# Performance work log

Measured on AMD Instinct MI355X. Metric: run time of the kernel, lower is better.

The kernel has to match this reference:

```python
import jax, jax.numpy as jnp
import numpy as np

B, S, D, H, P = 4, 2048, 1024, 16, 10
DK = D // H

def setup_inputs() -> dict:
    key = jax.random.key(0)
    ks = jax.random.split(key, 12)
    inp = {
        'q': jax.random.normal(ks[0], (B, S, D), jnp.float32),
        'k': jax.random.normal(ks[1], (B, S, D), jnp.float32),
        'v': jax.random.normal(ks[2], (B, S, D), jnp.float32),
        # causal mask, broadcastable over batch/heads
        'mask': jnp.tril(jnp.ones((S, S), jnp.int32))[None, None, :, :],
        'Wq': jax.random.normal(ks[3], (D, D), jnp.float32) * (1.0 / np.sqrt(D)),
        'bq': jnp.zeros((D,), jnp.float32),
        'Wk': jax.random.normal(ks[4], (D, D), jnp.float32) * (1.0 / np.sqrt(D)),
        'bk': jnp.zeros((D,), jnp.float32),
        'Wv': jax.random.normal(ks[5], (D, D), jnp.float32) * (1.0 / np.sqrt(D)),
        'bv': jnp.zeros((D,), jnp.float32),
        'Wo': jax.random.normal(ks[6], (D, D), jnp.float32) * (1.0 / np.sqrt(D)),
        'bo': jnp.zeros((D,), jnp.float32),
        'prefix_k': jax.random.normal(ks[7], (H, P, DK), jnp.float32) * 0.02,
        'prefix_v': jax.random.normal(ks[8], (H, P, DK), jnp.float32) * 0.02,
    }
    return inp

def reference(q, k, v, mask, Wq, bq, Wk, bk, Wv, bv, Wo, bo, prefix_k, prefix_v):
    bs, sq, d = q.shape
    h, p, dk = prefix_k.shape
    # projections -> [B, H, S, dk]
    Q = (q @ Wq + bq).reshape(bs, sq, h, dk).transpose(0, 2, 1, 3)
    K = (k @ Wk + bk).reshape(bs, -1, h, dk).transpose(0, 2, 1, 3)
    V = (v @ Wv + bv).reshape(bs, -1, h, dk).transpose(0, 2, 1, 3)
    # prepend learnable prefix K/V along the key axis
    pK = jnp.broadcast_to(prefix_k[None], (bs, h, p, dk))
    pV = jnp.broadcast_to(prefix_v[None], (bs, h, p, dk))
    K = jnp.concatenate([pK, K], axis=2)  # [B,H,P+S,dk]
    V = jnp.concatenate([pV, V], axis=2)
    # extend mask: prefix positions always visible
    pref_mask = jnp.ones(mask.shape[:3] + (p,), mask.dtype)
    full_mask = jnp.concatenate([pref_mask, mask], axis=-1)  # [.,.,S,P+S]
    scores = jnp.einsum('bhqd,bhkd->bhqk', Q, K) / np.sqrt(dk).astype(jnp.float32)
    scores = jnp.where(full_mask == 0, jnp.asarray(-1e9, scores.dtype), scores)
    attn = jax.nn.softmax(scores, axis=-1)  # dropout in eval mode: identity
    out = jnp.einsum('bhqk,bhkd->bhqd', attn, V)
    out = out.transpose(0, 2, 1, 3).reshape(bs, sq, d)
    return out @ Wo + bo
```

## Files before the change

kernel.cpp:

```cpp
#include <hip/hip_runtime.h>

typedef __bf16 bf16x8 __attribute__((ext_vector_type(8)));
typedef __bf16 bf16x4 __attribute__((ext_vector_type(4)));
typedef float f32x4 __attribute__((ext_vector_type(4)));

constexpr int Sq = 2048, Dd = 1024, Hn = 16, Pn = 10, DK = 64;
constexpr int SKPAD = 2112;
constexpr int NBH = 64;
constexpr float LOG2E = 1.44269504088896340736f;

__device__ __forceinline__ float exp2_fast(float x) {
  return __builtin_amdgcn_exp2f(x);
}

__device__ __forceinline__ unsigned short f2bf(float f) {
  unsigned int u = __float_as_uint(f);
  u += 0x7fffu + ((u >> 16) & 1u);
  return (unsigned short)(u >> 16);
}

__device__ __forceinline__ void gload_lds16(const void* g, void* l) {
  __builtin_amdgcn_global_load_lds(
      (const __attribute__((address_space(1))) void*)g,
      (__attribute__((address_space(3))) void*)l, 16, 0, 0);
}

__device__ __forceinline__ f32x4 mfma16(bf16x8 a, bf16x8 b, f32x4 c) {
  return __builtin_amdgcn_mfma_f32_16x16x32_bf16(a, b, c, 0, 0, 0);
}

__global__ void k_wt(const float* __restrict__ W0, const float* __restrict__ W1,
                     const float* __restrict__ W2, const float* __restrict__ W3,
                     unsigned short* __restrict__ T0, unsigned short* __restrict__ T1,
                     unsigned short* __restrict__ T2, unsigned short* __restrict__ T3) {
  __shared__ float tile[32][33];
  const float* W; unsigned short* T;
  switch (blockIdx.z) {
    case 0: W = W0; T = T0; break;
    case 1: W = W1; T = T1; break;
    case 2: W = W2; T = T2; break;
    default: W = W3; T = T3; break;
  }
  int n0 = blockIdx.x * 32, k0 = blockIdx.y * 32;
  int tx = threadIdx.x, ty = threadIdx.y;
  for (int r = ty; r < 32; r += 8)
    tile[r][tx] = W[(size_t)(k0 + r) * Dd + n0 + tx];
  __syncthreads();
  for (int r = ty; r < 32; r += 8)
    T[(size_t)(n0 + r) * Dd + k0 + tx] = f2bf(tile[tx][r]);
}

__global__ void k_fill(const float* __restrict__ pk, const float* __restrict__ pv,
                       unsigned short* __restrict__ Kb, unsigned short* __restrict__ Vt) {
  int bh = blockIdx.x;
  int h = bh & (Hn - 1);
  unsigned short* Kbh = Kb + (size_t)bh * SKPAD * DK;
  unsigned short* Vth = Vt + (size_t)bh * DK * SKPAD;
  for (int i = threadIdx.x; i < Pn * DK; i += blockDim.x) {
    int p = i >> 6, dk = i & 63;
    float kv = pk[((size_t)h * Pn + p) * DK + dk];
    float vv = pv[((size_t)h * Pn + p) * DK + dk];
    Kbh[(Sq + p) * DK + dk] = f2bf(kv);
    Vth[(size_t)dk * SKPAD + Sq + p] = f2bf(vv);
  }
  constexpr int ZR = SKPAD - (Pn + Sq);
  for (int i = threadIdx.x; i < ZR * DK; i += blockDim.x) {
    int r = i >> 6, c = i & 63;
    Kbh[(Sq + Pn + r) * DK + c] = 0;
    Vth[(size_t)c * SKPAD + (Sq + Pn + r)] = 0;
  }
}

__global__ __launch_bounds__(256, 3) void k_gemm_qkv(
    const float* __restrict__ Aq, const float* __restrict__ Ak,
    const float* __restrict__ Av,
    const unsigned short* __restrict__ Wq, const unsigned short* __restrict__ Wk,
    const unsigned short* __restrict__ Wv,
    const float* __restrict__ bq, const float* __restrict__ bk,
    const float* __restrict__ bv,
    unsigned short* __restrict__ Qo, unsigned short* __restrict__ Ko,
    unsigned short* __restrict__ Vo, float qscale) {
  __shared__ float Af[128 * 64];
  __shared__ unsigned short Bs[128 * 64];
  int bx0 = blockIdx.x;
  int orig = (bx0 & 7) * 192 + (bx0 >> 3);
  int stream = orig >> 9, within = orig & 511;

  const float* A32; const unsigned short* Bt; const float* bias;
  unsigned short* outB; float scale;
  switch (stream) {
    case 0:  A32 = Aq; Bt = Wq; bias = bq; outB = Qo; scale = qscale; break;
    case 1:  A32 = Ak; Bt = Wk; bias = bk; outB = Ko; scale = 1.f; break;
    default: A32 = Av; Bt = Wv; bias = bv; outB = Vo; scale = 1.f; break;
  }

  int tid = threadIdx.x;
  int w = tid >> 6, l = tid & 63;
  int lq = l & 15, lg = l >> 4;
  int tm = within >> 3, tn = within & 7;
  int brow = tm * 128, bcol = tn * 128;
  int wm = w >> 1, wn = w & 1;

  f32x4 acc[4][4];
#pragma unroll
  for (int m = 0; m < 4; ++m)
#pragma unroll
    for (int n = 0; n < 4; ++n) acc[m][n] = (f32x4){0.f, 0.f, 0.f, 0.f};

  for (int kt = 0; kt < 1024; kt += 64) {
#pragma unroll
    for (int it = 0; it < 8; ++it) {
      int c = it * 256 + tid;
      int row = c >> 4;
      int cb = (c & 15) * 16;
      int sb = cb ^ ((row & 7) << 4);
      gload_lds16((const char*)(A32 + (size_t)(brow + row) * 1024 + kt) + sb,
                  (char*)Af + (size_t)(it * 256 + w * 64) * 16);
    }
#pragma unroll
    for (int it = 0; it < 4; ++it) {
      int c = it * 256 + tid;
      int row = c >> 3;
      int cb = (c & 7) * 16;
      int sb = cb ^ ((row & 7) << 4);
      gload_lds16((const char*)(Bt + (size_t)(bcol + row) * 1024 + kt) + sb,
                  (char*)Bs + (size_t)(it * 256 + w * 64) * 16);
    }
    asm volatile("s_waitcnt vmcnt(0)" ::: "memory");
    __syncthreads();
#pragma unroll
    for (int ks = 0; ks < 2; ++ks) {
      bf16x8 af[4], bfv[4];
#pragma unroll
      for (int m = 0; m < 4; ++m) {
        int row = wm * 64 + m * 16 + lq;
        int b0 = row * 256 + ks * 128 + lg * 32;
        int sw = (row & 7) << 4;
        f32x4 a0 = *reinterpret_cast<const f32x4*>((const char*)Af + (b0 ^ sw));
        f32x4 a1 = *reinterpret_cast<const f32x4*>((const char*)Af + ((b0 + 16) ^ sw));
        bf16x8 v;
        v[0] = (__bf16)a0[0]; v[1] = (__bf16)a0[1];
        v[2] = (__bf16)a0[2]; v[3] = (__bf16)a0[3];
        v[4] = (__bf16)a1[0]; v[5] = (__bf16)a1[1];
        v[6] = (__bf16)a1[2]; v[7] = (__bf16)a1[3];
        af[m] = v;
      }
#pragma unroll
      for (int n = 0; n < 4; ++n) {
        int row = wn * 64 + n * 16 + lq;
        int byt = (row * 128 + ks * 64 + lg * 16) ^ ((row & 7) << 4);
        bfv[n] = *reinterpret_cast<const bf16x8*>((const char*)Bs + byt);
      }
#pragma unroll
      for (int m = 0; m < 4; ++m)
#pragma unroll
        for (int n = 0; n < 4; ++n)
          acc[m][n] = mfma16(af[m], bfv[n], acc[m][n]);
    }
    __syncthreads();
  }

  if (stream < 2) {
#pragma unroll
    for (int n = 0; n < 4; ++n) {
      int N = bcol + wn * 64 + n * 16 + lq;
      float bv = bias[N];
#pragma unroll
      for (int m = 0; m < 4; ++m) {
        int M0 = brow + wm * 64 + m * 16 + lg * 4;
#pragma unroll
        for (int r = 0; r < 4; ++r) {
          float val = (acc[m][n][r] + bv) * scale;
          int Mr = M0 + r;
          int b = Mr >> 11, s = Mr & 2047;
          int h = N >> 6, dk = N & 63;
          size_t idx;
          if (stream == 0) idx = (((size_t)(b * Hn + h)) * Sq + s) * DK + dk;
          else             idx = (((size_t)(b * Hn + h)) * SKPAD + s) * DK + dk;
          outB[idx] = f2bf(val);
        }
      }
    }
  } else {
    __syncthreads();
    unsigned short* T = (unsigned short*)Af;
#pragma unroll
    for (int n = 0; n < 4; ++n) {
      int col = wn * 64 + n * 16 + lq;
      float bv = bias[bcol + col];
      int sw = (col & 7) << 4;
#pragma unroll
      for (int m = 0; m < 4; ++m) {
        int row0 = wm * 64 + m * 16 + lg * 4;
        ushort4 p4;
        p4.x = f2bf(acc[m][n][0] + bv);
        p4.y = f2bf(acc[m][n][1] + bv);
        p4.z = f2bf(acc[m][n][2] + bv);
        p4.w = f2bf(acc[m][n][3] + bv);
        *reinterpret_cast<ushort4*>(&T[col * 128 + (row0 ^ sw)]) = p4;
      }
    }
    __syncthreads();
    int b = brow >> 11, s0 = brow & 2047;
    int col = tid >> 1;
    int off = (tid & 1) * 64;
    int sw = (col & 7) << 4;
    int h = (bcol + col) >> 6, dk = (bcol + col) & 63;
    unsigned short* dst = Vo + (((size_t)(b * Hn + h)) * DK + dk) * SKPAD + s0 + off;
#pragma unroll
    for (int j = 0; j < 8; ++j) {
      int4 v = *reinterpret_cast<const int4*>(&T[col * 128 + ((off + j * 8) ^ sw)]);
      *reinterpret_cast<int4*>(dst + j * 8) = v;
    }
  }
}

__global__ __launch_bounds__(256, 4) void k_gemm_o(
    const unsigned short* __restrict__ A, const unsigned short* __restrict__ Bt,
    const float* __restrict__ bias, float* __restrict__ outF) {
  __shared__ unsigned short As[128 * 64];
  __shared__ unsigned short Bs[128 * 64];
  int bx0 = blockIdx.x;
  int within = (bx0 & 7) * 64 + (bx0 >> 3);
  int tid = threadIdx.x;
  int w = tid >> 6, l = tid & 63;
  int lq = l & 15, lg = l >> 4;
  int tm = within >> 3, tn = within & 7;
  int brow = tm * 128, bcol = tn * 128;
  int wm = w >> 1, wn = w & 1;

  f32x4 acc[4][4];
#pragma unroll
  for (int m = 0; m < 4; ++m)
#pragma unroll
    for (int n = 0; n < 4; ++n) acc[m][n] = (f32x4){0.f, 0.f, 0.f, 0.f};

  for (int kt = 0; kt < 1024; kt += 64) {
#pragma unroll
    for (int it = 0; it < 4; ++it) {
      int c = it * 256 + tid;
      int row = c >> 3, col = c & 7;
      gload_lds16(A + (size_t)(brow + row) * 1024 + kt + col * 8,
                  As + (size_t)(it * 256 + w * 64) * 8);
      gload_lds16(Bt + (size_t)(bcol + row) * 1024 + kt + col * 8,
                  Bs + (size_t)(it * 256 + w * 64) * 8);
    }
    asm volatile("s_waitcnt vmcnt(0)" ::: "memory");
    __syncthreads();
    const bf16x8* As8 = reinterpret_cast<const bf16x8*>(As);
    const bf16x8* Bs8 = reinterpret_cast<const bf16x8*>(Bs);
#pragma unroll
    for (int ks = 0; ks < 2; ++ks) {
      bf16x8 af[4], bfv[4];
#pragma unroll
      for (int m = 0; m < 4; ++m)
        af[m] = As8[(size_t)(wm * 64 + m * 16 + lq) * 8 + ks * 4 + lg];
#pragma unroll
      for (int n = 0; n < 4; ++n)
        bfv[n] = Bs8[(size_t)(wn * 64 + n * 16 + lq) * 8 + ks * 4 + lg];
#pragma unroll
      for (int m = 0; m < 4; ++m)
#pragma unroll
        for (int n = 0; n < 4; ++n)
          acc[m][n] = mfma16(af[m], bfv[n], acc[m][n]);
    }
    __syncthreads();
  }

#pragma unroll
  for (int n = 0; n < 4; ++n) {
    int N = bcol + wn * 64 + n * 16 + lq;
    float bv = bias[N];
#pragma unroll
    for (int m = 0; m < 4; ++m) {
      int M0 = brow + wm * 64 + m * 16 + lg * 4;
#pragma unroll
      for (int r = 0; r < 4; ++r)
        outF[(size_t)(M0 + r) * 1024 + N] = acc[m][n][r] + bv;
    }
  }
}

__global__ __launch_bounds__(256, 4) void k_attn(
    const unsigned short* __restrict__ Qb, const unsigned short* __restrict__ Kb,
    const unsigned short* __restrict__ Vt, unsigned short* __restrict__ O) {
  __shared__ unsigned short Ks[2][64 * 64];
  __shared__ unsigned short Vs[2][64 * 64];
  __shared__ unsigned short Ps[4][16 * 64];
  int tid = threadIdx.x;
  int w = tid >> 6, l = tid & 63;
  int lq = l & 15, lg = l >> 4;
  int bh = blockIdx.x;
  int pi = blockIdx.y;
  int qtL = pi, qtH = 31 - pi;
  int ntot = qtH + 2;
  int qsA[2] = {qtL * 64, qtH * 64};

  bf16x8 qf[2][2];
#pragma unroll
  for (int qt = 0; qt < 2; ++qt) {
    const unsigned short* Qg = Qb + ((size_t)bh * Sq + qsA[qt] + w * 16) * DK;
#pragma unroll
    for (int ks = 0; ks < 2; ++ks)
      qf[qt][ks] = *reinterpret_cast<const bf16x8*>(
          Qg + (size_t)lq * DK + ks * 32 + lg * 8);
  }

  const unsigned short* Kg = Kb + (size_t)bh * SKPAD * DK;
  const unsigned short* Vg = Vt + (size_t)bh * DK * SKPAD;

  float m_run[2] = {-1e30f, -1e30f};
  float l_part[2] = {0.f, 0.f};
  f32x4 oacc[2][4];
#pragma unroll
  for (int qt = 0; qt < 2; ++qt)
#pragma unroll
    for (int n = 0; n < 4; ++n) oacc[qt][n] = (f32x4){0.f, 0.f, 0.f, 0.f};

  unsigned short* Pw = &Ps[w][0];

  auto STAGE = [&](int b, int tile) {
    int kt = tile * 64;
#pragma unroll
    for (int it = 0; it < 2; ++it) {
      int dst = (it * 256 + tid) * 16;
      int srcK = dst ^ (((dst >> 7) & 7) << 4);
      gload_lds16((const char*)(Kg + (size_t)kt * DK) + srcK,
                  (char*)Ks[b] + (size_t)(it * 256 + w * 64) * 16);
    }
#pragma unroll
    for (int it = 0; it < 2; ++it) {
      int dst = (it * 256 + tid) * 16;
      int row = dst >> 7;
      int colb = (dst & 127) ^ ((row & 7) << 4);
      gload_lds16((const char*)(Vg + (size_t)row * SKPAD + kt) + colb,
                  (char*)Vs[b] + (size_t)(it * 256 + w * 64) * 16);
    }
  };

  STAGE(0, 0);
  asm volatile("s_waitcnt vmcnt(0)" ::: "memory");
  __syncthreads();

  for (int t = 0; t < ntot; ++t) {
    int bsel = t & 1;
    bool isLast = (t == ntot - 1);
    if (!isLast) STAGE(bsel ^ 1, (t + 1 == ntot - 1) ? (Sq / 64) : (t + 1));
    int kt = isLast ? Sq : t * 64;

#pragma unroll
    for (int qt = 0; qt < 2; ++qt) {
      int qs = qsA[qt];
      if (!isLast) {
        if (qt == 0 && t > qtL) continue;
        if (kt > qs + w * 16 + 15) continue;
      }

      f32x4 st[4];
#pragma unroll
      for (int m = 0; m < 4; ++m) st[m] = (f32x4){0.f, 0.f, 0.f, 0.f};
      __builtin_amdgcn_s_setprio(1);
#pragma unroll
      for (int ks = 0; ks < 2; ++ks) {
#pragma unroll
        for (int m = 0; m < 4; ++m) {
          if (isLast && m > 0) continue;
          int krow = m * 16 + lq;
          int byt = (krow * 128 + ks * 64 + lg * 16) ^ ((krow & 7) << 4);
          bf16x8 kf = *reinterpret_cast<const bf16x8*>((const char*)Ks[bsel] + byt);
          st[m] = mfma16(kf, qf[qt][ks], st[m]);
        }
      }
      __builtin_amdgcn_s_setprio(0);

      if (isLast) {
#pragma unroll
        for (int m = 0; m < 4; ++m)
#pragma unroll
          for (int r = 0; r < 4; ++r) {
            int ki = m * 16 + lg * 4 + r;
            st[m][r] = (ki < Pn) ? st[m][r] : -1e30f;
          }
      } else if (kt + 63 > qs + w * 16) {
        int qrow = qs + w * 16 + lq;
#pragma unroll
        for (int m = 0; m < 4; ++m)
#pragma unroll
          for (int r = 0; r < 4; ++r) {
            int key = kt + m * 16 + lg * 4 + r;
            st[m][r] = (key <= qrow) ? st[m][r] : -1e30f;
          }
      }

      float mx = fmaxf(fmaxf(st[0][0], st[0][1]), fmaxf(st[0][2], st[0][3]));
#pragma unroll
      for (int m = 1; m < 4; ++m)
        mx = fmaxf(mx, fmaxf(fmaxf(st[m][0], st[m][1]), fmaxf(st[m][2], st[m][3])));
      if (__any(mx > m_run[qt] + 8.f)) {
        float gmx = fmaxf(mx, __shfl_xor(mx, 16));
        gmx = fmaxf(gmx, __shfl_xor(gmx, 32));
        float mnew = fmaxf(m_run[qt], gmx);
        float alpha = exp2_fast(m_run[qt] - mnew);
        m_run[qt] = mnew;
        l_part[qt] *= alpha;
        float ar[4];
#pragma unroll
        for (int r = 0; r < 4; ++r) ar[r] = __shfl(alpha, lg * 4 + r);
#pragma unroll
        for (int n = 0; n < 4; ++n)
#pragma unroll
          for (int r = 0; r < 4; ++r) oacc[qt][n][r] *= ar[r];
      }
      float rs = 0.f;
#pragma unroll
      for (int m = 0; m < 4; ++m) {
        bf16x4 p4;
#pragma unroll
        for (int r = 0; r < 4; ++r) {
          float p = exp2_fast(st[m][r] - m_run[qt]);
          rs += p;
          p4[r] = (__bf16)p;
        }
        int byt = (lq * 128 + m * 32 + lg * 8) ^ ((lq & 7) << 4);
        *reinterpret_cast<bf16x4*>((char*)Pw + byt) = p4;
      }
      l_part[qt] += rs;

      __builtin_amdgcn_s_setprio(1);
#pragma unroll
      for (int ks = 0; ks < 2; ++ks) {
        if (isLast && ks == 1) continue;
        int pbyt = (lq * 128 + ks * 64 + lg * 16) ^ ((lq & 7) << 4);
        bf16x8 pf = *reinterpret_cast<const bf16x8*>((const char*)Pw + pbyt);
#pragma unroll
        for (int n = 0; n < 4; ++n) {
          int dv = n * 16 + lq;
          int vbyt = (dv * 128 + ks * 64 + lg * 16) ^ ((dv & 7) << 4);
          bf16x8 vf = *reinterpret_cast<const bf16x8*>((const char*)Vs[bsel] + vbyt);
          oacc[qt][n] = mfma16(pf, vf, oacc[qt][n]);
        }
      }
      __builtin_amdgcn_s_setprio(0);
    }
    asm volatile("s_waitcnt vmcnt(0)" ::: "memory");
    __syncthreads();
  }

  int b = bh >> 4, h = bh & 15;
#pragma unroll
  for (int qt = 0; qt < 2; ++qt) {
    float ls = l_part[qt];
    ls += __shfl_xor(ls, 16);
    ls += __shfl_xor(ls, 32);
    float lr[4];
#pragma unroll
    for (int r = 0; r < 4; ++r) lr[r] = 1.0f / __shfl(ls, lg * 4 + r);
#pragma unroll
    for (int n = 0; n < 4; ++n)
#pragma unroll
      for (int r = 0; r < 4; ++r) {
        int qrow2 = qsA[qt] + w * 16 + lg * 4 + r;
        size_t idx = ((size_t)b * Sq + qrow2) * Dd + h * DK + n * 16 + lq;
        O[idx] = f2bf(oacc[qt][n][r] * lr[r]);
      }
  }
}

extern "C" void kernel_launch(void* const* d_in, const int* in_sizes, int n_in,
                              void* d_out, int out_size, void* d_ws, size_t ws_size,
                              hipStream_t stream) {
  (void)in_sizes; (void)n_in; (void)out_size; (void)ws_size;
  const float* q  = (const float*)d_in[0];
  const float* k  = (const float*)d_in[1];
  const float* v  = (const float*)d_in[2];
  const float* Wq = (const float*)d_in[4];
  const float* bq = (const float*)d_in[5];
  const float* Wk = (const float*)d_in[6];
  const float* bk = (const float*)d_in[7];
  const float* Wv = (const float*)d_in[8];
  const float* bv = (const float*)d_in[9];
  const float* Wo = (const float*)d_in[10];
  const float* bo = (const float*)d_in[11];
  const float* pk = (const float*)d_in[12];
  const float* pv = (const float*)d_in[13];

  unsigned short* wsp = (unsigned short*)d_ws;
  size_t off = 0;
  auto take = [&](size_t elems) { unsigned short* p = wsp + off; off += elems; return p; };
  unsigned short* Ob  = take(8388608);
  unsigned short* wqt = take(1048576);
  unsigned short* wkt = take(1048576);
  unsigned short* wvt = take(1048576);
  unsigned short* wot = take(1048576);
  unsigned short* Qbf = take(8388608);
  unsigned short* KbB = take((size_t)NBH * SKPAD * DK);
  unsigned short* VtB = take((size_t)NBH * DK * SKPAD);
  float* outF = (float*)d_out;

  k_wt<<<dim3(32, 32, 4), dim3(32, 8), 0, stream>>>(Wq, Wk, Wv, Wo, wqt, wkt, wvt, wot);
  k_fill<<<64, 256, 0, stream>>>(pk, pv, KbB, VtB);
  k_gemm_qkv<<<1536, 256, 0, stream>>>(q, k, v, wqt, wkt, wvt,
                                       bq, bk, bv, Qbf, KbB, VtB,
                                       0.125f * LOG2E);
  k_attn<<<dim3(NBH, 16), 256, 0, stream>>>(Qbf, KbB, VtB, Ob);
  k_gemm_o<<<512, 256, 0, stream>>>(Ob, wot, bo, outF);
}
```

Baseline: 185.7 us.

## Prefetch fp32 A tile into registers and stage it as bf16 in LDS

In the QKV projection GEMM, the next fp32 A tile is now loaded into registers while the MFMAs for the current tile run. Each element is converted to bf16 once and written to a swizzled bf16 LDS tile, instead of staging fp32 in LDS and converting on every fragment read. This halves LDS use for A, which may allow more resident blocks, and removes the duplicated conversion across waves. In exchange it adds register pressure from the prefetch buffers. The B tile is now stored and read without the XOR swizzle, which risks LDS bank conflicts.

```diff
diff --git a/kernel.cpp b/kernel.cpp
--- a/kernel.cpp
+++ b/kernel.cpp
@@ -80,8 +80,9 @@
     const float* __restrict__ bv,
     unsigned short* __restrict__ Qo, unsigned short* __restrict__ Ko,
     unsigned short* __restrict__ Vo, float qscale) {
-  __shared__ float Af[128 * 64];
-  __shared__ unsigned short Bs[128 * 64];
+  __shared__ unsigned short S[2 * 128 * 64];
+  unsigned short* As = S;
+  unsigned short* Bs = S + 128 * 64;
   int bx0 = blockIdx.x;
   int orig = (bx0 & 7) * 192 + (bx0 >> 3);
   int stream = orig >> 9, within = orig & 511;
@@ -107,55 +108,74 @@
 #pragma unroll
     for (int n = 0; n < 4; ++n) acc[m][n] = (f32x4){0.f, 0.f, 0.f, 0.f};
 
-  for (int kt = 0; kt < 1024; kt += 64) {
-#pragma unroll
-    for (int it = 0; it < 8; ++it) {
-      int c = it * 256 + tid;
-      int row = c >> 4;
-      int cb = (c & 15) * 16;
-      int sb = cb ^ ((row & 7) << 4);
-      gload_lds16((const char*)(A32 + (size_t)(brow + row) * 1024 + kt) + sb,
-                  (char*)Af + (size_t)(it * 256 + w * 64) * 16);
-    }
+  float4 aLo[4], aRg[4];
+  auto LOADA = [&](int kt) {
+#pragma unroll
+    for (int it = 0; it < 4; ++it) {
+      int idx = it * 256 + tid;
+      int row = idx >> 3, col8 = idx & 7;
+      const float* src = A32 + (size_t)(brow + row) * 1024 + kt + col8 * 8;
+      aLo[it] = *reinterpret_cast<const float4*>(src);
+      aRg[it] = *reinterpret_cast<const float4*>(src + 4);
+    }
+  };
+  auto CVTW = [&]() {
+#pragma unroll
+    for (int it = 0; it < 4; ++it) {
+      int idx = it * 256 + tid;
+      int row = idx >> 3, col8 = idx & 7;
+      bf16x8 v;
+      v[0] = (__bf16)aLo[it].x; v[1] = (__bf16)aLo[it].y;
+      v[2] = (__bf16)aLo[it].z; v[3] = (__bf16)aLo[it].w;
+      v[4] = (__bf16)aRg[it].x; v[5] = (__bf16)aRg[it].y;
+      v[6] = (__bf16)aRg[it].z; v[7] = (__bf16)aRg[it].w;
+      int byt = (row * 128 + col8 * 16) ^ ((row & 7) << 4);
+      *reinterpret_cast<bf16x8*>((char*)As + byt) = v;
+    }
+  };
+  auto GLOADB = [&](int kt) {
 #pragma unroll
     for (int it = 0; it < 4; ++it) {
       int c = it * 256 + tid;
-      int row = c >> 3;
-      int cb = (c & 7) * 16;
-      int sb = cb ^ ((row & 7) << 4);
-      gload_lds16((const char*)(Bt + (size_t)(bcol + row) * 1024 + kt) + sb,
-                  (char*)Bs + (size_t)(it * 256 + w * 64) * 16);
-    }
-    asm volatile("s_waitcnt vmcnt(0)" ::: "memory");
-    __syncthreads();
+      int row = c >> 3, col = c & 7;
+      gload_lds16(Bt + (size_t)(bcol + row) * 1024 + kt + col * 8,
+                  Bs + (size_t)(it * 256 + w * 64) * 8);
+    }
+  };
+
+  LOADA(0);
+  GLOADB(0);
+  CVTW();
+  asm volatile("s_waitcnt vmcnt(0)" ::: "memory");
+  __syncthreads();
+
+  for (int kt = 0; kt < 1024; kt += 64) {
+    bool more = (kt + 64) < 1024;
+    if (more) LOADA(kt + 64);
+    const bf16x8* Bs8 = reinterpret_cast<const bf16x8*>(Bs);
 #pragma unroll
     for (int ks = 0; ks < 2; ++ks) {
       bf16x8 af[4], bfv[4];
 #pragma unroll
       for (int m = 0; m < 4; ++m) {
         int row = wm * 64 + m * 16 + lq;
-        int b0 = row * 256 + ks * 128 + lg * 32;
-        int sw = (row & 7) << 4;
-        f32x4 a0 = *reinterpret_cast<const f32x4*>((const char*)Af + (b0 ^ sw));
-        f32x4 a1 = *reinterpret_cast<const f32x4*>((const char*)Af + ((b0 + 16) ^ sw));
-        bf16x8 v;
-        v[0] = (__bf16)a0[0]; v[1] = (__bf16)a0[1];
-        v[2] = (__bf16)a0[2]; v[3] = (__bf16)a0[3];
-        v[4] = (__bf16)a1[0]; v[5] = (__bf16)a1[1];
-        v[6] = (__bf16)a1[2]; v[7] = (__bf16)a1[3];
-        af[m] = v;
-      }
-#pragma unroll
-      for (int n = 0; n < 4; ++n) {
-        int row = wn * 64 + n * 16 + lq;
         int byt = (row * 128 + ks * 64 + lg * 16) ^ ((row & 7) << 4);
-        bfv[n] = *reinterpret_cast<const bf16x8*>((const char*)Bs + byt);
-      }
+        af[m] = *reinterpret_cast<const bf16x8*>((const char*)As + byt);
+      }
+#pragma unroll
+      for (int n = 0; n < 4; ++n)
+        bfv[n] = Bs8[(size_t)(wn * 64 + n * 16 + lq) * 8 + ks * 4 + lg];
 #pragma unroll
       for (int m = 0; m < 4; ++m)
 #pragma unroll
         for (int n = 0; n < 4; ++n)
           acc[m][n] = mfma16(af[m], bfv[n], acc[m][n]);
+    }
+    __syncthreads();
+    if (more) {
+      GLOADB(kt + 64);
+      CVTW();
+      asm volatile("s_waitcnt vmcnt(0)" ::: "memory");
     }
     __syncthreads();
   }
@@ -183,7 +203,7 @@
     }
   } else {
     __syncthreads();
-    unsigned short* T = (unsigned short*)Af;
+    unsigned short* T = S;
 #pragma unroll
     for (int n = 0; n < 4; ++n) {
       int col = wn * 64 + n * 16 + lq;
```

Result: no change. 187.5 us (+1.0%).

## Load GEMM weight fragments directly from global memory, shrink O-GEMM tile to 64 rows

Applied to the files above, without the earlier changes.

In both the QKV and output projection GEMMs, the weight operand is no longer staged through LDS. Each wave reads its bf16 weight fragments straight from global memory (relying on L2/cache reuse), which cuts LDS use and allows higher occupancy (QKV launch bounds raised to 4). The output GEMM also moves to 64x128 tiles with 1024 blocks and adds an XOR swizzle to its A staging. The cost is uncoalesced, higher-latency global loads inside the inner loop that are not overlapped with compute, and redundant weight reads across waves.

```diff
diff --git a/kernel.cpp b/kernel.cpp
--- a/kernel.cpp
+++ b/kernel.cpp
@@ -71,7 +71,7 @@
   }
 }
 
-__global__ __launch_bounds__(256, 3) void k_gemm_qkv(
+__global__ __launch_bounds__(256, 4) void k_gemm_qkv(
     const float* __restrict__ Aq, const float* __restrict__ Ak,
     const float* __restrict__ Av,
     const unsigned short* __restrict__ Wq, const unsigned short* __restrict__ Wk,
@@ -81,7 +81,6 @@
     unsigned short* __restrict__ Qo, unsigned short* __restrict__ Ko,
     unsigned short* __restrict__ Vo, float qscale) {
   __shared__ float Af[128 * 64];
-  __shared__ unsigned short Bs[128 * 64];
   int bx0 = blockIdx.x;
   int orig = (bx0 & 7) * 192 + (bx0 >> 3);
   int stream = orig >> 9, within = orig & 511;
@@ -112,25 +111,20 @@
     for (int it = 0; it < 8; ++it) {
       int c = it * 256 + tid;
       int row = c >> 4;
-      int cb = (c & 15) * 16;
-      int sb = cb ^ ((row & 7) << 4);
+      int sb = ((c & 15) * 16) ^ ((row & 7) << 4);
       gload_lds16((const char*)(A32 + (size_t)(brow + row) * 1024 + kt) + sb,
                   (char*)Af + (size_t)(it * 256 + w * 64) * 16);
     }
-#pragma unroll
-    for (int it = 0; it < 4; ++it) {
-      int c = it * 256 + tid;
-      int row = c >> 3;
-      int cb = (c & 7) * 16;
-      int sb = cb ^ ((row & 7) << 4);
-      gload_lds16((const char*)(Bt + (size_t)(bcol + row) * 1024 + kt) + sb,
-                  (char*)Bs + (size_t)(it * 256 + w * 64) * 16);
-    }
     asm volatile("s_waitcnt vmcnt(0)" ::: "memory");
     __syncthreads();
 #pragma unroll
     for (int ks = 0; ks < 2; ++ks) {
-      bf16x8 af[4], bfv[4];
+      bf16x8 bfv[4];
+#pragma unroll
+      for (int n = 0; n < 4; ++n)
+        bfv[n] = *reinterpret_cast<const bf16x8*>(
+            Bt + (size_t)(bcol + wn * 64 + n * 16 + lq) * 1024 + kt + ks * 32 + lg * 8);
+      bf16x8 af[4];
 #pragma unroll
       for (int m = 0; m < 4; ++m) {
         int row = wm * 64 + m * 16 + lq;
@@ -146,12 +140,6 @@
         af[m] = v;
       }
 #pragma unroll
-      for (int n = 0; n < 4; ++n) {
-        int row = wn * 64 + n * 16 + lq;
-        int byt = (row * 128 + ks * 64 + lg * 16) ^ ((row & 7) << 4);
-        bfv[n] = *reinterpret_cast<const bf16x8*>((const char*)Bs + byt);
-      }
-#pragma unroll
       for (int m = 0; m < 4; ++m)
 #pragma unroll
         for (int n = 0; n < 4; ++n)
@@ -218,48 +206,49 @@
 __global__ __launch_bounds__(256, 4) void k_gemm_o(
     const unsigned short* __restrict__ A, const unsigned short* __restrict__ Bt,
     const float* __restrict__ bias, float* __restrict__ outF) {
-  __shared__ unsigned short As[128 * 64];
-  __shared__ unsigned short Bs[128 * 64];
+  __shared__ unsigned short As[64 * 64];
   int bx0 = blockIdx.x;
-  int within = (bx0 & 7) * 64 + (bx0 >> 3);
+  int within = (bx0 & 7) * 128 + (bx0 >> 3);
   int tid = threadIdx.x;
   int w = tid >> 6, l = tid & 63;
   int lq = l & 15, lg = l >> 4;
   int tm = within >> 3, tn = within & 7;
-  int brow = tm * 128, bcol = tn * 128;
+  int brow = tm * 64, bcol = tn * 128;
   int wm = w >> 1, wn = w & 1;
 
-  f32x4 acc[4][4];
-#pragma unroll
-  for (int m = 0; m < 4; ++m)
+  f32x4 acc[2][4];
+#pragma unroll
+  for (int m = 0; m < 2; ++m)
 #pragma unroll
     for (int n = 0; n < 4; ++n) acc[m][n] = (f32x4){0.f, 0.f, 0.f, 0.f};
 
   for (int kt = 0; kt < 1024; kt += 64) {
 #pragma unroll
-    for (int it = 0; it < 4; ++it) {
+    for (int it = 0; it < 2; ++it) {
       int c = it * 256 + tid;
-      int row = c >> 3, col = c & 7;
-      gload_lds16(A + (size_t)(brow + row) * 1024 + kt + col * 8,
-                  As + (size_t)(it * 256 + w * 64) * 8);
-      gload_lds16(Bt + (size_t)(bcol + row) * 1024 + kt + col * 8,
-                  Bs + (size_t)(it * 256 + w * 64) * 8);
+      int row = c >> 3;
+      int sb = ((c & 7) * 16) ^ ((row & 7) << 4);
+      gload_lds16((const char*)(A + (size_t)(brow + row) * 1024 + kt) + sb,
+                  (char*)As + (size_t)(it * 256 + w * 64) * 16);
     }
     asm volatile("s_waitcnt vmcnt(0)" ::: "memory");
     __syncthreads();
-    const bf16x8* As8 = reinterpret_cast<const bf16x8*>(As);
-    const bf16x8* Bs8 = reinterpret_cast<const bf16x8*>(Bs);
 #pragma unroll
     for (int ks = 0; ks < 2; ++ks) {
-      bf16x8 af[4], bfv[4];
-#pragma unroll
-      for (int m = 0; m < 4; ++m)
-        af[m] = As8[(size_t)(wm * 64 + m * 16 + lq) * 8 + ks * 4 + lg];
+      bf16x8 bfv[4];
 #pragma unroll
       for (int n = 0; n < 4; ++n)
-        bfv[n] = Bs8[(size_t)(wn * 64 + n * 16 + lq) * 8 + ks * 4 + lg];
-#pragma unroll
-      for (int m = 0; m < 4; ++m)
+        bfv[n] = *reinterpret_cast<const bf16x8*>(
+            Bt + (size_t)(bcol + wn * 64 + n * 16 + lq) * 1024 + kt + ks * 32 + lg * 8);
+      bf16x8 af[2];
+#pragma unroll
+      for (int m = 0; m < 2; ++m) {
+        int row = wm * 32 + m * 16 + lq;
+        int byt = (row * 128 + ks * 64 + lg * 16) ^ ((row & 7) << 4);
+        af[m] = *reinterpret_cast<const bf16x8*>((const char*)As + byt);
+      }
+#pragma unroll
+      for (int m = 0; m < 2; ++m)
 #pragma unroll
         for (int n = 0; n < 4; ++n)
           acc[m][n] = mfma16(af[m], bfv[n], acc[m][n]);
@@ -272,8 +261,8 @@
     int N = bcol + wn * 64 + n * 16 + lq;
     float bv = bias[N];
 #pragma unroll
-    for (int m = 0; m < 4; ++m) {
-      int M0 = brow + wm * 64 + m * 16 + lg * 4;
+    for (int m = 0; m < 2; ++m) {
+      int M0 = brow + wm * 32 + m * 16 + lg * 4;
 #pragma unroll
       for (int r = 0; r < 4; ++r)
         outF[(size_t)(M0 + r) * 1024 + N] = acc[m][n][r] + bv;
@@ -326,7 +315,7 @@
       int dst = (it * 256 + tid) * 16;
       int srcK = dst ^ (((dst >> 7) & 7) << 4);
       gload_lds16((const char*)(Kg + (size_t)kt * DK) + srcK,
-                  (char*)Ks[b] + (size_t)(it * 256 + w * 64) * 16);
+                  (char*)&Ks[b][0] + (size_t)(it * 256 + w * 64) * 16);
     }
 #pragma unroll
     for (int it = 0; it < 2; ++it) {
@@ -334,7 +323,7 @@
       int row = dst >> 7;
       int colb = (dst & 127) ^ ((row & 7) << 4);
       gload_lds16((const char*)(Vg + (size_t)row * SKPAD + kt) + colb,
-                  (char*)Vs[b] + (size_t)(it * 256 + w * 64) * 16);
+                  (char*)&Vs[b][0] + (size_t)(it * 256 + w * 64) * 16);
     }
   };
 
@@ -367,7 +356,7 @@
           if (isLast && m > 0) continue;
           int krow = m * 16 + lq;
           int byt = (krow * 128 + ks * 64 + lg * 16) ^ ((krow & 7) << 4);
-          bf16x8 kf = *reinterpret_cast<const bf16x8*>((const char*)Ks[bsel] + byt);
+          bf16x8 kf = *reinterpret_cast<const bf16x8*>((const char*)&Ks[bsel][0] + byt);
           st[m] = mfma16(kf, qf[qt][ks], st[m]);
         }
       }
@@ -436,7 +425,7 @@
         for (int n = 0; n < 4; ++n) {
           int dv = n * 16 + lq;
           int vbyt = (dv * 128 + ks * 64 + lg * 16) ^ ((dv & 7) << 4);
-          bf16x8 vf = *reinterpret_cast<const bf16x8*>((const char*)Vs[bsel] + vbyt);
+          bf16x8 vf = *reinterpret_cast<const bf16x8*>((const char*)&Vs[bsel][0] + vbyt);
           oacc[qt][n] = mfma16(pf, vf, oacc[qt][n]);
         }
       }
@@ -503,5 +492,5 @@
                                        bq, bk, bv, Qbf, KbB, VtB,
                                        0.125f * LOG2E);
   k_attn<<<dim3(NBH, 16), 256, 0, stream>>>(Qbf, KbB, VtB, Ob);
-  k_gemm_o<<<512, 256, 0, stream>>>(Ob, wot, bo, outF);
-}
+  k_gemm_o<<<1024, 256, 0, stream>>>(Ob, wot, bo, outF);
+}
```

After: 276.6 us. 48.9% more time.
